# Performance work log

Hardware: AMD Instinct MI355X
Metric: run time of the kernel (lower is better)

## Reference

```python
import jax, jax.numpy as jnp
import numpy as np

# --- dims (match init_kwargs) ---
B, IN_DIM, OUT_DIM, CAUSES_DIM = 4096, 512, 4096, 256
POOL = 2
N_STEPS = 10
GAMMA = 0.1
LR = 0.001  # fixed lr inside _IstaStep
S = int(np.sqrt(OUT_DIM))   # 64: side of the square code map
SP = S // POOL              # 32: pooled side
POOLED_DIM = SP * SP        # 1024: second dim of V (pool path)


def setup_inputs() -> dict:
    key = jax.random.key(0)
    k1, k2, k3 = jax.random.split(key, 3)
    inputs = jax.random.normal(k1, (B, IN_DIM), jnp.float32)
    limit = float(np.sqrt(6.0 / (OUT_DIM + IN_DIM)))  # glorot_uniform for W
    W = jax.random.uniform(k2, (OUT_DIM, IN_DIM), jnp.float32, -limit, limit)
    # pool_flag=True -> V ~ U(0, 1) with shape (causes_dim, pooled_dim)
    V = jax.random.uniform(k3, (CAUSES_DIM, POOLED_DIM), jnp.float32, 0.0, 1.0)
    return {"inputs": inputs, "W": W, "V": V}


def _soft_threshold(x, t):
    # _proxOp: max(x - t, 0) + min(x + t, 0)
    return jnp.maximum(x - t, 0.0) + jnp.minimum(x + t, 0.0)


def reference(inputs, W, V):
    Bn = inputs.shape[0]
    x0 = jnp.zeros((Bn, OUT_DIM), inputs.dtype)
    u0 = jnp.full((Bn, CAUSES_DIM), 0.1, inputs.dtype)   # zeros + 0.1
    rec0 = jnp.zeros((Bn, IN_DIM), inputs.dtype)

    def step(carry, _):
        x, u, _rec = carry
        outputs = x @ W                                   # [B, IN_DIM], linear activation
        # NOTE: original uses (1 + exp(-z)) * 0.5 (not a true sigmoid) — keep faithful
        causes = (1.0 + jnp.exp(-(u @ V))) * 0.5          # [B, POOLED_DIM]
        # nearest-neighbor upsample of the pooled cause map back to the code map
        causes_up = jnp.repeat(
            jnp.repeat(causes.reshape(Bn, SP, SP), POOL, axis=1), POOL, axis=2
        ).reshape(Bn, OUT_DIM)                            # [B, OUT_DIM]
        # T.grad(sum((inputs - x@W)^2), x) = 2 * (x@W - inputs) @ W.T
        grad_x = 2.0 * (outputs - inputs) @ W.T           # [B, OUT_DIM]
        # prior=0 in _get_output, so the _proxInnov branch is dead code
        x_new = jax.lax.stop_gradient(                    # disconnected_grad
            _soft_threshold(x - LR * grad_x, LR * GAMMA * causes_up))
        # 2x2 max pool over the square code map
        x_pool = x_new.reshape(Bn, SP, POOL, SP, POOL).max(axis=(2, 4)).reshape(Bn, POOLED_DIM)
        # T.grad(sum(causes(u) * x_pool * gamma), u): d causes/dz = -0.5*exp(-z)
        dcauses = -0.5 * jnp.exp(-(u @ V))                # [B, POOLED_DIM]
        grad_u = (dcauses * x_pool * GAMMA) @ V.T         # [B, CAUSES_DIM]
        u_new = jax.lax.stop_gradient(
            _soft_threshold(u - LR * grad_u, LR * GAMMA / 10.0))
        return (x_new, u_new, outputs), None

    (x, u, rec), _ = jax.lax.scan(step, (x0, u0, rec0), None, length=N_STEPS)
    # return_mode='rec': reconstruction computed in the last step (from x_{T-1})
    return rec
```

## Files before the change

kernel.cpp:

```cpp
#include <hip/hip_runtime.h>
#include <math.h>


#define NB 4096
#define IN_DIM 512
#define OUT_DIM 4096
#define CAUSES_DIM 256
#define POOLED_DIM 1024

typedef __attribute__((ext_vector_type(8))) short short8;
typedef __attribute__((ext_vector_type(4))) float f32x4;

static constexpr float LR = 0.001f;
static constexpr float GAMMA = 0.1f;

enum { EP_R = 0, EP_OUT, EP_UUP };

__device__ __forceinline__ float softthr(float v, float t) {
    return fmaxf(v - t, 0.0f) + fminf(v + t, 0.0f);
}
__device__ __forceinline__ unsigned short f2bf(float f) {
    unsigned int u = __builtin_bit_cast(unsigned int, f);
    u = (u + 0x7fffu + ((u >> 16) & 1u)) >> 16;
    return (unsigned short)u;
}
__device__ __forceinline__ float bf2f(unsigned short h) {
    return __builtin_bit_cast(float, (unsigned int)h << 16);
}
__device__ __forceinline__ void gload_lds16(const unsigned short* g, unsigned short* l) {
    __builtin_amdgcn_global_load_lds(
        (const __attribute__((address_space(1))) void*)g,
        (__attribute__((address_space(3))) void*)l, 16, 0, 0);
}

template<int ROWS, int K>
__device__ __forceinline__ void stage_tile(const unsigned short* __restrict__ g,
                                           unsigned short* l, int row0, int k0, int t)
{
#pragma unroll
    for (int j = 0; j < ROWS / 32; j++) {
        const int idx = j * 256 + t;
        const int row = idx >> 3;
        const int sl  = (idx & 7) ^ (row & 7);
        gload_lds16(g + (size_t)(row0 + row) * K + k0 + sl * 8,
                    l + (size_t)(idx & ~63) * 8);
    }
}

template<int BM, int BN, int K>
__device__ __forceinline__ void kloop2(unsigned short* lds,
    const unsigned short* __restrict__ A, const unsigned short* __restrict__ B,
    int m0, int n0, f32x4 (&acc)[BM / 32][BN / 32])
{
    constexpr int FM = BM / 32, FN = BN / 32;
    constexpr int NK = K / 64, ST = (BM + BN) * 64, L = (BM + BN) / 32;
    static_assert(NK >= 2, "pipeline needs >=2 K-tiles");
    const int t = threadIdx.x;
    const int lane = t & 63, wid = t >> 6;
    const int l15 = lane & 15, l7 = lane & 7, g = lane >> 4;
    const int wm0 = (wid >> 1) * (BM / 2), wn0 = (wid & 1) * (BN / 2);

    auto stage = [&](int s, int b) {
        stage_tile<BM, K>(A, lds + b * ST, m0, s * 64, t);
        stage_tile<BN, K>(B, lds + b * ST + BM * 64, n0, s * 64, t);
    };
    auto comp = [&](int b) {
        const unsigned short* As = lds + b * ST;
        const unsigned short* Bs = lds + b * ST + BM * 64;
#pragma unroll
        for (int ks = 0; ks < 2; ks++) {
            const int so = (((ks * 4) + g) ^ l7) * 8;
            short8 af[FM], bfv[FN];
#pragma unroll
            for (int fi = 0; fi < FM; fi++)
                af[fi] = *(const short8*)&As[(wm0 + fi * 16 + l15) * 64 + so];
#pragma unroll
            for (int fj = 0; fj < FN; fj++)
                bfv[fj] = *(const short8*)&Bs[(wn0 + fj * 16 + l15) * 64 + so];
#pragma unroll
            for (int fi = 0; fi < FM; fi++)
#pragma unroll
                for (int fj = 0; fj < FN; fj++)
                    acc[fi][fj] = __builtin_amdgcn_mfma_f32_16x16x32_bf16(
                        af[fi], bfv[fj], acc[fi][fj], 0, 0, 0);
        }
    };

    stage(0, 0); stage(1, 1);
    int b = 0;
#pragma unroll 1
    for (int i = 0; i < NK - 1; ++i) {
        asm volatile("s_waitcnt vmcnt(%0)" :: "n"(L) : "memory");
        __builtin_amdgcn_s_barrier();
        comp(b);
        __builtin_amdgcn_s_barrier();
        if (i + 2 < NK) stage(i + 2, b);
        b ^= 1;
    }
    asm volatile("s_waitcnt vmcnt(0)" ::: "memory");
    __builtin_amdgcn_s_barrier();
    comp(b);
}

template<int BM, int BN, int N, int K, int EP>
__device__ void gemm_core(unsigned short* lds, int m0, int n0,
                          const unsigned short* __restrict__ A,
                          const unsigned short* __restrict__ B,
                          const float* __restrict__ auxf,
                          void* __restrict__ out0, void* __restrict__ out1)
{
    constexpr int FM = BM / 32, FN = BN / 32;
    const int t = threadIdx.x, lane = t & 63, wid = t >> 6;
    const int l15 = lane & 15, g = lane >> 4;
    const int wm0 = (wid >> 1) * (BM / 2), wn0 = (wid & 1) * (BN / 2);

    f32x4 acc[FM][FN];
#pragma unroll
    for (int fi = 0; fi < FM; fi++)
#pragma unroll
        for (int fj = 0; fj < FN; fj++) acc[fi][fj] = (f32x4){0.f, 0.f, 0.f, 0.f};

    kloop2<BM, BN, K>(lds, A, B, m0, n0, acc);

#pragma unroll
    for (int fi = 0; fi < FM; fi++) {
#pragma unroll
        for (int fj = 0; fj < FN; fj++) {
#pragma unroll
            for (int r = 0; r < 4; r++) {
                const int row = m0 + wm0 + fi * 16 + g * 4 + r;
                const int col = n0 + wn0 + fj * 16 + l15;
                const float v = acc[fi][fj][r];
                if (EP == EP_R) {
                    ((unsigned short*)out0)[(size_t)row * N + col] =
                        f2bf(v - auxf[(size_t)row * N + col]);
                } else if (EP == EP_OUT) {
                    ((float*)out0)[(size_t)row * N + col] = v;
                } else {
                    float* up = (float*)out0;
                    const size_t idx = (size_t)row * CAUSES_DIM + col;
                    const float uv = softthr(up[idx] - LR * v, LR * GAMMA * 0.1f);
                    up[idx] = uv;
                    ((unsigned short*)out1)[idx] = f2bf(uv);
                }
            }
        }
    }
}

template<bool FIRST, bool POOLF>
__global__ __launch_bounds__(256)
void xupc_kernel(const unsigned short* __restrict__ Rbf,
                 const unsigned short* __restrict__ Wbf,
                 const unsigned short* __restrict__ ubf,
                 const unsigned short* __restrict__ VTbf,
                 unsigned short* __restrict__ xbf,
                 unsigned short* __restrict__ gbf)
{
    constexpr int BM = 128, BN = 128;
    __shared__ unsigned short lds[2 * (BM + BN) * 64 + 8192];
    unsigned* czdc = (unsigned*)(lds + 2 * (BM + BN) * 64);
    unsigned short* xs = lds;

    const int t = threadIdx.x, lane = t & 63, wid = t >> 6;
    const int l15 = lane & 15, g = lane >> 4;
    const int xcd = blockIdx.x & 7, l = blockIdx.x >> 3;
    const int g2 = l >> 5, r2 = l & 31;
    const int bm = g2 * 8 + (r2 >> 2), bn = xcd * 4 + (r2 & 3);
    const int m0 = bm * BM, n0 = bn * BN;
    const int wm0 = (wid >> 1) * 64, wn0 = (wid & 1) * 64;

    f32x4 acc[4][4];
#pragma unroll
    for (int fi = 0; fi < 4; fi++)
#pragma unroll
        for (int fj = 0; fj < 4; fj++) acc[fi][fj] = (f32x4){0.f, 0.f, 0.f, 0.f};
    kloop2<128, 128, IN_DIM>(lds, Rbf, Wbf, m0, n0, acc);
    __syncthreads();

    f32x4 zacc[4][1];
#pragma unroll
    for (int fi = 0; fi < 4; fi++) zacc[fi][0] = (f32x4){0.f, 0.f, 0.f, 0.f};
    kloop2<128, 32, CAUSES_DIM>(lds, ubf, VTbf, m0, bn * 32, zacc);

    {
        const int zc = (wid & 1) * 16 + l15;
#pragma unroll
        for (int fi = 0; fi < 4; fi++) {
#pragma unroll
            for (int r = 0; r < 4; r++) {
                const int zr = (wid >> 1) * 64 + fi * 16 + g * 4 + r;
                const float e = expf(-zacc[fi][0][r]);
                czdc[zr * 32 + zc] =
                    (unsigned)f2bf(0.5f + 0.5f * e) | ((unsigned)f2bf(-0.5f * e) << 16);
            }
        }
    }
    __syncthreads();

#pragma unroll
    for (int fi = 0; fi < 4; fi++) {
#pragma unroll
        for (int fj = 0; fj < 4; fj++) {
#pragma unroll
            for (int r = 0; r < 4; r++) {
                const int rloc = wm0 + fi * 16 + g * 4 + r;
                const int cloc = wn0 + fj * 16 + l15;
                const int pl = (cloc & 63) >> 1;
                const float cz = bf2f((unsigned short)(czdc[rloc * 32 + pl] & 0xffffu));
                const size_t idx = (size_t)(m0 + rloc) * OUT_DIM + n0 + cloc;
                const float xold = FIRST ? 0.0f : bf2f(xbf[idx]);
                const float xv = softthr(xold - 2.0f * LR * acc[fi][fj][r],
                                         LR * GAMMA * cz);
                const unsigned short xq = f2bf(xv);
                xbf[idx] = xq;
                if (POOLF) xs[rloc * 130 + cloc] = xq;
            }
        }
    }

    if (POOLF) {
        __syncthreads();
        const int p = t & 31;
        const int rbase = (t >> 5) * 16;
#pragma unroll
        for (int i = 0; i < 16; i++) {
            const int prow = rbase + i;
            const unsigned short* xr = &xs[prow * 130 + 2 * p];
            const float mx = fmaxf(fmaxf(bf2f(xr[0]), bf2f(xr[1])),
                                   fmaxf(bf2f(xr[64]), bf2f(xr[65])));
            const float dcv = bf2f((unsigned short)(czdc[prow * 32 + p] >> 16));
            gbf[(size_t)(m0 + prow) * POOLED_DIM + bn * 32 + p] = f2bf(dcv * mx * GAMMA);
        }
    }
}

__global__ __launch_bounds__(256)
void h_uup_r_kernel(const unsigned short* __restrict__ gbf,
                    const unsigned short* __restrict__ Vbf,
                    float* __restrict__ u, unsigned short* __restrict__ ubf,
                    const unsigned short* __restrict__ xbf,
                    const unsigned short* __restrict__ WTbf,
                    const float* __restrict__ inputs,
                    unsigned short* __restrict__ Rbf)
{
    __shared__ unsigned short lds[2 * (128 + 64) * 64];
    if (blockIdx.x < 256) {
        const int bid = blockIdx.x;
        gemm_core<128, 64, IN_DIM, OUT_DIM, EP_R>(
            lds, (bid >> 3) * 128, (bid & 7) * 64, xbf, WTbf, inputs, Rbf, nullptr);
    } else {
        const int bid = blockIdx.x - 256;
        gemm_core<64, 64, CAUSES_DIM, POOLED_DIM, EP_UUP>(
            lds, (bid >> 2) * 64, (bid & 3) * 64, gbf, Vbf, nullptr, u, ubf);
    }
}

__global__ __launch_bounds__(256)
void out_kernel(const unsigned short* __restrict__ xbf,
                const unsigned short* __restrict__ WTbf,
                float* __restrict__ out)
{
    __shared__ unsigned short lds[2 * (128 + 64) * 64];
    const int bid = blockIdx.x;
    gemm_core<128, 64, IN_DIM, OUT_DIM, EP_OUT>(
        lds, (bid >> 3) * 128, (bid & 7) * 64, xbf, WTbf, nullptr, out, nullptr);
}

__global__ __launch_bounds__(256)
void prep_k(const float* __restrict__ in, unsigned short* __restrict__ direct,
            unsigned short* __restrict__ transp, int R, int C)
{
    __shared__ float tile[32][33];
    const int bx = blockIdx.x * 32, by = blockIdx.y * 32;
    const int tx = threadIdx.x % 32, ty = threadIdx.x / 32;
#pragma unroll
    for (int i = 0; i < 32; i += 8) {
        const float v = in[(size_t)(by + ty + i) * C + bx + tx];
        tile[ty + i][tx] = v;
        direct[(size_t)(by + ty + i) * C + bx + tx] = f2bf(v);
    }
    __syncthreads();
#pragma unroll
    for (int i = 0; i < 32; i += 8)
        transp[(size_t)(bx + ty + i) * R + by + tx] = f2bf(tile[tx][ty + i]);
}

__global__ void negcast_k(const float* __restrict__ in, unsigned short* __restrict__ out,
                          int n4)
{
    const int i = blockIdx.x * 256 + threadIdx.x;
    if (i >= n4) return;
    float4 v = ((const float4*)in)[i];
    union { unsigned short s[4]; unsigned long long u; } p;
    p.s[0] = f2bf(-v.x); p.s[1] = f2bf(-v.y); p.s[2] = f2bf(-v.z); p.s[3] = f2bf(-v.w);
    ((unsigned long long*)out)[i] = p.u;
}

__global__ void fill_u_k(float* __restrict__ u, unsigned short* __restrict__ ubf, int n) {
    const int i = blockIdx.x * 256 + threadIdx.x;
    if (i >= n) return;
    u[i] = 0.1f;
    ubf[i] = f2bf(0.1f);
}

extern "C" void kernel_launch(void* const* d_in, const int* in_sizes, int n_in,
                              void* d_out, int out_size, void* d_ws, size_t ws_size,
                              hipStream_t stream)
{
    const float* inputs = (const float*)d_in[0];
    const float* W      = (const float*)d_in[1];
    const float* V      = (const float*)d_in[2];
    float* out = (float*)d_out;

    char* w = (char*)d_ws;
    unsigned short* xbf  = (unsigned short*)w; w += (size_t)NB * OUT_DIM * 2;
    unsigned short* Rbf  = (unsigned short*)w; w += (size_t)NB * IN_DIM * 2;
    unsigned short* gbf  = (unsigned short*)w; w += (size_t)NB * POOLED_DIM * 2;
    float*          u    = (float*)w;          w += (size_t)NB * CAUSES_DIM * 4;
    unsigned short* ubf  = (unsigned short*)w; w += (size_t)NB * CAUSES_DIM * 2;
    unsigned short* Wbf  = (unsigned short*)w; w += (size_t)OUT_DIM * IN_DIM * 2;
    unsigned short* WTbf = (unsigned short*)w; w += (size_t)OUT_DIM * IN_DIM * 2;
    unsigned short* Vbf  = (unsigned short*)w; w += (size_t)CAUSES_DIM * POOLED_DIM * 2;
    unsigned short* VTbf = (unsigned short*)w;

    prep_k<<<dim3(IN_DIM / 32, OUT_DIM / 32), 256, 0, stream>>>(W, Wbf, WTbf, OUT_DIM, IN_DIM);
    prep_k<<<dim3(POOLED_DIM / 32, CAUSES_DIM / 32), 256, 0, stream>>>(V, Vbf, VTbf, CAUSES_DIM, POOLED_DIM);
    fill_u_k<<<NB * CAUSES_DIM / 256, 256, 0, stream>>>(u, ubf, NB * CAUSES_DIM);
    negcast_k<<<NB * IN_DIM / 4 / 256, 256, 0, stream>>>(inputs, Rbf, NB * IN_DIM / 4);

    xupc_kernel<true, true><<<1024, 256, 0, stream>>>(Rbf, Wbf, ubf, VTbf, xbf, gbf);
    h_uup_r_kernel<<<512, 256, 0, stream>>>(gbf, Vbf, u, ubf, xbf, WTbf, inputs, Rbf);
    for (int t = 1; t < 8; t++) {
        xupc_kernel<false, true><<<1024, 256, 0, stream>>>(Rbf, Wbf, ubf, VTbf, xbf, gbf);
        h_uup_r_kernel<<<512, 256, 0, stream>>>(gbf, Vbf, u, ubf, xbf, WTbf, inputs, Rbf);
    }
    xupc_kernel<false, false><<<1024, 256, 0, stream>>>(Rbf, Wbf, ubf, VTbf, xbf, gbf);
    out_kernel<<<256, 256, 0, stream>>>(xbf, WTbf, out);
}
```

Before: 819.6 us.

## Use triple-buffered LDS K-loop and XCD-aware block remap for x@W^T GEMMs

Replaces the double-buffered K-loop with a three-stage LDS pipeline, so two tiles of global->LDS loads stay in flight while one is computed. It also remaps block IDs in the R and output GEMMs so that blocks landing on the same XCD share A-row tiles, which should improve L2 reuse. The cost is 1.5x more LDS per block (72KB), which can lower occupancy. The smaller EP_UUP GEMM (K=1024) also goes through the new loop.

```diff
diff --git a/kernel.cpp b/kernel.cpp
--- a/kernel.cpp
+++ b/kernel.cpp
@@ -45,6 +45,65 @@
         gload_lds16(g + (size_t)(row0 + row) * K + k0 + sl * 8,
                     l + (size_t)(idx & ~63) * 8);
     }
+}
+
+template<int BM, int BN, int K>
+__device__ __forceinline__ void kloop3(unsigned short* lds,
+    const unsigned short* __restrict__ A, const unsigned short* __restrict__ B,
+    int m0, int n0, f32x4 (&acc)[BM / 32][BN / 32])
+{
+    constexpr int FM = BM / 32, FN = BN / 32;
+    constexpr int NK = K / 64, ST = (BM + BN) * 64, L = (BM + BN) / 32;
+    static_assert(NK >= 3, "pipeline needs >=3 K-tiles");
+    const int t = threadIdx.x;
+    const int lane = t & 63, wid = t >> 6;
+    const int l15 = lane & 15, l7 = lane & 7, g = lane >> 4;
+    const int wm0 = (wid >> 1) * (BM / 2), wn0 = (wid & 1) * (BN / 2);
+
+    auto stage = [&](int s, int b) {
+        stage_tile<BM, K>(A, lds + b * ST, m0, s * 64, t);
+        stage_tile<BN, K>(B, lds + b * ST + BM * 64, n0, s * 64, t);
+    };
+    auto comp = [&](int b) {
+        const unsigned short* As = lds + b * ST;
+        const unsigned short* Bs = lds + b * ST + BM * 64;
+#pragma unroll
+        for (int ks = 0; ks < 2; ks++) {
+            const int so = (((ks * 4) + g) ^ l7) * 8;
+            short8 af[FM], bfv[FN];
+#pragma unroll
+            for (int fi = 0; fi < FM; fi++)
+                af[fi] = *(const short8*)&As[(wm0 + fi * 16 + l15) * 64 + so];
+#pragma unroll
+            for (int fj = 0; fj < FN; fj++)
+                bfv[fj] = *(const short8*)&Bs[(wn0 + fj * 16 + l15) * 64 + so];
+#pragma unroll
+            for (int fi = 0; fi < FM; fi++)
+#pragma unroll
+                for (int fj = 0; fj < FN; fj++)
+                    acc[fi][fj] = __builtin_amdgcn_mfma_f32_16x16x32_bf16(
+                        af[fi], bfv[fj], acc[fi][fj], 0, 0, 0);
+        }
+    };
+
+    stage(0, 0); stage(1, 1); stage(2, 2);
+    int b = 0;
+#pragma unroll 1
+    for (int i = 0; i < NK - 2; ++i) {
+        asm volatile("s_waitcnt vmcnt(%0)" :: "n"(2 * L) : "memory");
+        __builtin_amdgcn_s_barrier();
+        comp(b);
+        __builtin_amdgcn_s_barrier();
+        if (i + 3 < NK) stage(i + 3, b);
+        b = (b == 2) ? 0 : b + 1;
+    }
+    asm volatile("s_waitcnt vmcnt(%0)" :: "n"(L) : "memory");
+    __builtin_amdgcn_s_barrier();
+    comp(b);
+    b = (b == 2) ? 0 : b + 1;
+    asm volatile("s_waitcnt vmcnt(0)" ::: "memory");
+    __builtin_amdgcn_s_barrier();
+    comp(b);
 }
 
 template<int BM, int BN, int K>
@@ -120,7 +179,7 @@
 #pragma unroll
         for (int fj = 0; fj < FN; fj++) acc[fi][fj] = (f32x4){0.f, 0.f, 0.f, 0.f};
 
-    kloop2<BM, BN, K>(lds, A, B, m0, n0, acc);
+    kloop3<BM, BN, K>(lds, A, B, m0, n0, acc);
 
 #pragma unroll
     for (int fi = 0; fi < FM; fi++) {
@@ -244,11 +303,14 @@
                     const float* __restrict__ inputs,
                     unsigned short* __restrict__ Rbf)
 {
-    __shared__ unsigned short lds[2 * (128 + 64) * 64];
+    __shared__ unsigned short lds[3 * (128 + 64) * 64];
     if (blockIdx.x < 256) {
         const int bid = blockIdx.x;
+        const int xcd = bid & 7, l = bid >> 3;
+        const int bm = xcd * 4 + (l >> 3);
+        const int bn = l & 7;
         gemm_core<128, 64, IN_DIM, OUT_DIM, EP_R>(
-            lds, (bid >> 3) * 128, (bid & 7) * 64, xbf, WTbf, inputs, Rbf, nullptr);
+            lds, bm * 128, bn * 64, xbf, WTbf, inputs, Rbf, nullptr);
     } else {
         const int bid = blockIdx.x - 256;
         gemm_core<64, 64, CAUSES_DIM, POOLED_DIM, EP_UUP>(
@@ -261,10 +323,13 @@
                 const unsigned short* __restrict__ WTbf,
                 float* __restrict__ out)
 {
-    __shared__ unsigned short lds[2 * (128 + 64) * 64];
+    __shared__ unsigned short lds[3 * (128 + 64) * 64];
     const int bid = blockIdx.x;
+    const int xcd = bid & 7, l = bid >> 3;
+    const int bm = xcd * 4 + (l >> 3);
+    const int bn = l & 7;
     gemm_core<128, 64, IN_DIM, OUT_DIM, EP_OUT>(
-        lds, (bid >> 3) * 128, (bid & 7) * 64, xbf, WTbf, nullptr, out, nullptr);
+        lds, bm * 128, bn * 64, xbf, WTbf, nullptr, out, nullptr);
 }
 
 __global__ __launch_bounds__(256)
```

Result: faster. 737.1 us (-10.1%).

## Prefetch LDS fragments before next-stage load, enlarge R/out tiles with XCD mapping

Applied to the files above, without the earlier changes.

The K-loop now reads all LDS fragments for a tile into registers, waits on lgkmcnt, and then issues the next global stage before running the MFMAs at raised wave priority. This lets global loads overlap with matrix math, and the epilogue iteration is folded into the loop. The R and output GEMMs move from 128x64 to 128x128 tiles with an XCD-aware block mapping, halving their block counts. The cost is higher register pressure from the doubled fragment arrays and more LDS per block. With only 128 large-tile blocks, the R/out GEMMs may underfill the GPU's CUs.

```diff
diff --git a/kernel.cpp b/kernel.cpp
--- a/kernel.cpp
+++ b/kernel.cpp
@@ -64,42 +64,52 @@
         stage_tile<BM, K>(A, lds + b * ST, m0, s * 64, t);
         stage_tile<BN, K>(B, lds + b * ST + BM * 64, n0, s * 64, t);
     };
-    auto comp = [&](int b) {
+
+    short8 af[2][FM], bfv[2][FN];
+    auto readfrags = [&](int b) {
         const unsigned short* As = lds + b * ST;
         const unsigned short* Bs = lds + b * ST + BM * 64;
 #pragma unroll
         for (int ks = 0; ks < 2; ks++) {
             const int so = (((ks * 4) + g) ^ l7) * 8;
-            short8 af[FM], bfv[FN];
 #pragma unroll
             for (int fi = 0; fi < FM; fi++)
-                af[fi] = *(const short8*)&As[(wm0 + fi * 16 + l15) * 64 + so];
+                af[ks][fi] = *(const short8*)&As[(wm0 + fi * 16 + l15) * 64 + so];
 #pragma unroll
             for (int fj = 0; fj < FN; fj++)
-                bfv[fj] = *(const short8*)&Bs[(wn0 + fj * 16 + l15) * 64 + so];
+                bfv[ks][fj] = *(const short8*)&Bs[(wn0 + fj * 16 + l15) * 64 + so];
+        }
+    };
+    auto mfma_all = [&]() {
+        __builtin_amdgcn_s_setprio(1);
+#pragma unroll
+        for (int ks = 0; ks < 2; ks++)
 #pragma unroll
             for (int fi = 0; fi < FM; fi++)
 #pragma unroll
                 for (int fj = 0; fj < FN; fj++)
                     acc[fi][fj] = __builtin_amdgcn_mfma_f32_16x16x32_bf16(
-                        af[fi], bfv[fj], acc[fi][fj], 0, 0, 0);
-        }
+                        af[ks][fi], bfv[ks][fj], acc[fi][fj], 0, 0, 0);
+        __builtin_amdgcn_s_setprio(0);
     };
 
     stage(0, 0); stage(1, 1);
     int b = 0;
 #pragma unroll 1
-    for (int i = 0; i < NK - 1; ++i) {
-        asm volatile("s_waitcnt vmcnt(%0)" :: "n"(L) : "memory");
+    for (int i = 0; i < NK; ++i) {
+        if (i < NK - 1)
+            asm volatile("s_waitcnt vmcnt(%0)" :: "n"(L) : "memory");
+        else
+            asm volatile("s_waitcnt vmcnt(0)" ::: "memory");
         __builtin_amdgcn_s_barrier();
-        comp(b);
+        readfrags(b);
+        asm volatile("s_waitcnt lgkmcnt(0)" ::: "memory");
+        __builtin_amdgcn_sched_barrier(0);
         __builtin_amdgcn_s_barrier();
         if (i + 2 < NK) stage(i + 2, b);
+        mfma_all();
         b ^= 1;
     }
-    asm volatile("s_waitcnt vmcnt(0)" ::: "memory");
-    __builtin_amdgcn_s_barrier();
-    comp(b);
 }
 
 template<int BM, int BN, int N, int K, int EP>
@@ -244,13 +254,16 @@
                     const float* __restrict__ inputs,
                     unsigned short* __restrict__ Rbf)
 {
-    __shared__ unsigned short lds[2 * (128 + 64) * 64];
-    if (blockIdx.x < 256) {
+    __shared__ unsigned short lds[2 * (128 + 128) * 64];
+    if (blockIdx.x < 128) {
         const int bid = blockIdx.x;
-        gemm_core<128, 64, IN_DIM, OUT_DIM, EP_R>(
-            lds, (bid >> 3) * 128, (bid & 7) * 64, xbf, WTbf, inputs, Rbf, nullptr);
+        const int xcd = bid & 7, l = bid >> 3;
+        const int bm = xcd * 4 + (l >> 2);
+        const int bn = l & 3;
+        gemm_core<128, 128, IN_DIM, OUT_DIM, EP_R>(
+            lds, bm * 128, bn * 128, xbf, WTbf, inputs, Rbf, nullptr);
     } else {
-        const int bid = blockIdx.x - 256;
+        const int bid = blockIdx.x - 128;
         gemm_core<64, 64, CAUSES_DIM, POOLED_DIM, EP_UUP>(
             lds, (bid >> 2) * 64, (bid & 3) * 64, gbf, Vbf, nullptr, u, ubf);
     }
@@ -261,10 +274,13 @@
                 const unsigned short* __restrict__ WTbf,
                 float* __restrict__ out)
 {
-    __shared__ unsigned short lds[2 * (128 + 64) * 64];
+    __shared__ unsigned short lds[2 * (128 + 128) * 64];
     const int bid = blockIdx.x;
-    gemm_core<128, 64, IN_DIM, OUT_DIM, EP_OUT>(
-        lds, (bid >> 3) * 128, (bid & 7) * 64, xbf, WTbf, nullptr, out, nullptr);
+    const int xcd = bid & 7, l = bid >> 3;
+    const int bm = xcd * 4 + (l >> 2);
+    const int bn = l & 3;
+    gemm_core<128, 128, IN_DIM, OUT_DIM, EP_OUT>(
+        lds, bm * 128, bn * 128, xbf, WTbf, nullptr, out, nullptr);
 }
 
 __global__ __launch_bounds__(256)
@@ -330,11 +346,11 @@
     negcast_k<<<NB * IN_DIM / 4 / 256, 256, 0, stream>>>(inputs, Rbf, NB * IN_DIM / 4);
 
     xupc_kernel<true, true><<<1024, 256, 0, stream>>>(Rbf, Wbf, ubf, VTbf, xbf, gbf);
-    h_uup_r_kernel<<<512, 256, 0, stream>>>(gbf, Vbf, u, ubf, xbf, WTbf, inputs, Rbf);
+    h_uup_r_kernel<<<384, 256, 0, stream>>>(gbf, Vbf, u, ubf, xbf, WTbf, inputs, Rbf);
     for (int t = 1; t < 8; t++) {
         xupc_kernel<false, true><<<1024, 256, 0, stream>>>(Rbf, Wbf, ubf, VTbf, xbf, gbf);
-        h_uup_r_kernel<<<512, 256, 0, stream>>>(gbf, Vbf, u, ubf, xbf, WTbf, inputs, Rbf);
+        h_uup_r_kernel<<<384, 256, 0, stream>>>(gbf, Vbf, u, ubf, xbf, WTbf, inputs, Rbf);
     }
     xupc_kernel<false, false><<<1024, 256, 0, stream>>>(Rbf, Wbf, ubf, VTbf, xbf, gbf);
-    out_kernel<<<256, 256, 0, stream>>>(xbf, WTbf, out);
-}
+    out_kernel<<<128, 256, 0, stream>>>(xbf, WTbf, out);
+}
```

After: 771.3 us. 1.06x faster.
